# Kernel tuning notes

Measured on AMD Instinct MI355X. Metric: run time of the kernel, lower is better.

## Reference

```python
import jax, jax.numpy as jnp
import numpy as np

N = 100000      # nodes
E = 1600000     # edges
NODE_DIM = 128
HID = 128
L = 3           # num_layers
B = 512         # graphs in batch
EPS = 1e-5      # LayerNorm eps


def setup_inputs() -> dict:
    key = jax.random.key(0)
    ks = jax.random.split(key, 8)
    nodes = jax.random.normal(ks[0], (N, NODE_DIM), jnp.float32)
    edges = jax.random.randint(ks[1], (2, E), 0, N, dtype=jnp.int32)
    edge_types = jax.random.randint(ks[2], (E,), 0, 10, dtype=jnp.int32)
    batch_idx = jnp.sort(jax.random.randint(ks[3], (N,), 0, B, dtype=jnp.int32))
    w_in = jax.random.normal(ks[4], (NODE_DIM, HID), jnp.float32) / np.sqrt(NODE_DIM)
    b_in = jnp.zeros((HID,), jnp.float32)
    gcn_w = jax.random.normal(ks[5], (L, HID, HID), jnp.float32) / np.sqrt(HID)
    gcn_b = jnp.zeros((L, HID), jnp.float32)
    ln_g = jnp.ones((L, HID), jnp.float32)
    ln_b = jnp.zeros((L, HID), jnp.float32)
    return {"nodes": nodes, "edges": edges, "edge_types": edge_types,
            "batch_idx": batch_idx, "w_in": w_in, "b_in": b_in,
            "gcn_w": gcn_w, "gcn_b": gcn_b, "ln_g": ln_g, "ln_b": ln_b}


def _layer_norm(x, g, b):
    mu = jnp.mean(x, axis=-1, keepdims=True)
    var = jnp.mean(jnp.square(x - mu), axis=-1, keepdims=True)
    return (x - mu) * jax.lax.rsqrt(var + EPS) * g + b


def reference(nodes, edges, edge_types, batch_idx, w_in, b_in, gcn_w, gcn_b, ln_g, ln_b):
    src, dst = edges[0], edges[1]
    # GCN normalization with self-loops: deg = in-degree(A) + 1
    deg = jax.ops.segment_sum(jnp.ones((E,), nodes.dtype), dst, num_segments=N) + 1.0
    dinv_sqrt = jax.lax.rsqrt(deg)
    dinv = 1.0 / deg                       # self-loop norm = 1/deg_i
    enorm = dinv_sqrt[src] * dinv_sqrt[dst]

    x = nodes @ w_in + b_in                # input projection [N, HID]
    for i in range(L):
        res = x
        xw = x @ gcn_w[i]
        agg = jax.ops.segment_sum(xw[src] * enorm[:, None], dst, num_segments=N)
        x = agg + xw * dinv[:, None] + gcn_b[i]
        x = jax.nn.relu(_layer_norm(x, ln_g[i], ln_b[i]))
        # dropout is identity in eval mode
        if i > 0:
            x = x + res                    # residual only for i > 0

    # global mean pool per graph
    counts = jax.ops.segment_sum(jnp.ones((N,), x.dtype), batch_idx, num_segments=B)
    plan = jax.ops.segment_sum(x, batch_idx, num_segments=B) / jnp.maximum(counts, 1.0)[:, None]
    return x, plan
```

## Files before the change

kernel.cpp:

```cpp
#include <hip/hip_runtime.h>
#include <hip/hip_bf16.h>

typedef __attribute__((ext_vector_type(8))) short bf16x8;
typedef __attribute__((ext_vector_type(4))) float f32x4;
typedef __attribute__((ext_vector_type(2))) float f32x2;

#define K1_TILE 6144
#define NBCAP 4608

__device__ __forceinline__ unsigned short f2bf(float f) {
    union { unsigned int i; float f; } x; x.f = f;
    unsigned int r = (x.i + 0x7fffu + ((x.i >> 16) & 1u)) >> 16;
    return (unsigned short)r;
}
__device__ __forceinline__ float blo(unsigned int u) { return __uint_as_float(u << 16); }
__device__ __forceinline__ float bhi(unsigned int u) { return __uint_as_float(u & 0xffff0000u); }


__global__ __launch_bounds__(256) void bin2_k(const int* __restrict__ src,
                                              const int* __restrict__ dst,
                                              int* __restrict__ bucket_cursor,
                                              int* __restrict__ bins,
                                              int E, int NB) {
    __shared__ int hist[512];
    __shared__ int lbase[513];
    __shared__ int gdiff[512];
    __shared__ int wsum[4];
    __shared__ int stage[K1_TILE];
    int tid = threadIdx.x;
    int base = blockIdx.x * K1_TILE;
    int cnt = min(K1_TILE, E - base);

    hist[tid] = 0; hist[tid + 256] = 0;
    __syncthreads();
    for (int i = tid; i < cnt; i += 256) atomicAdd(&hist[dst[base + i] >> 8], 1);
    __syncthreads();

    int h0 = hist[2 * tid], h1 = hist[2 * tid + 1];
    int v = h0 + h1;
    int lane = tid & 63, wid = tid >> 6;
    int s = v;
#pragma unroll
    for (int o = 1; o < 64; o <<= 1) { int n = __shfl_up(s, o); if (lane >= o) s += n; }
    if (lane == 63) wsum[wid] = s;
    __syncthreads();
    if (tid == 0) { int r = 0; for (int w = 0; w < 4; ++w) { int t2 = wsum[w]; wsum[w] = r; r += t2; } }
    __syncthreads();
    int lb0 = s + wsum[wid] - v;
    int lb1 = lb0 + h0;
    int b0 = 2 * tid, b1 = 2 * tid + 1;
    int gb0 = 0, gb1 = 0;
    if (h0 > 0 && b0 < NB) gb0 = atomicAdd(&bucket_cursor[b0], h0);
    if (h1 > 0 && b1 < NB) gb1 = atomicAdd(&bucket_cursor[b1], h1);
    __syncthreads();
    hist[b0] = lb0; hist[b1] = lb1;
    lbase[b0] = lb0; lbase[b1] = lb1;
    gdiff[b0] = gb0 - lb0; gdiff[b1] = gb1 - lb1;
    if (tid == 0) lbase[512] = cnt;
    __syncthreads();

    for (int i = tid; i < cnt; i += 256) {
        int sv = src[base + i], dv = dst[base + i];
        int pos = atomicAdd(&hist[dv >> 8], 1);
        stage[pos] = ((dv & 255) << 24) | sv;
    }
    __syncthreads();

    for (int i = tid; i < cnt; i += 256) {
        int lo = 0, hi = 512;
        while (lo + 1 < hi) { int mid = (lo + hi) >> 1; if (lbase[mid] <= i) lo = mid; else hi = mid; }
        int p = gdiff[lo] + i;
        if (p < NBCAP) bins[(size_t)lo * NBCAP + p] = stage[i];
    }
}


__global__ __launch_bounds__(256) void bucket_scan_k(const int* __restrict__ bucket_cursor,
                                                     int* __restrict__ bucket_base, int NB) {
    __shared__ int wsum[4];
    int tid = threadIdx.x;
    int h0 = (2 * tid < NB) ? min(bucket_cursor[2 * tid], NBCAP) : 0;
    int h1 = (2 * tid + 1 < NB) ? min(bucket_cursor[2 * tid + 1], NBCAP) : 0;
    int v = h0 + h1;
    int lane = tid & 63, wid = tid >> 6;
    int s = v;
#pragma unroll
    for (int o = 1; o < 64; o <<= 1) { int n = __shfl_up(s, o); if (lane >= o) s += n; }
    if (lane == 63) wsum[wid] = s;
    __syncthreads();
    if (tid == 0) { int r = 0; for (int w = 0; w < 4; ++w) { int t2 = wsum[w]; wsum[w] = r; r += t2; } }
    __syncthreads();
    int excl = s + wsum[wid] - v;
    if (2 * tid < NB) bucket_base[2 * tid] = excl;
    if (2 * tid + 1 < NB) bucket_base[2 * tid + 1] = excl + h0;
}


__global__ __launch_bounds__(256) void csr_build_k(const int* __restrict__ bins,
                                                   const int* __restrict__ bucket_cursor,
                                                   const int* __restrict__ bucket_base,
                                                   int* __restrict__ csr_src,
                                                   int* __restrict__ row_start,
                                                   float* __restrict__ dinv_sqrt,
                                                   float* __restrict__ dinv,
                                                   int N) {
    __shared__ int counts[256];
    __shared__ int cursor[256];
    __shared__ int wsum[4];
    __shared__ int lcsr[NBCAP];
    int b = blockIdx.x, tid = threadIdx.x;
    int cnt = min(bucket_cursor[b], NBCAP);
    int cbase = bucket_base[b];
    const int* my = bins + (size_t)b * NBCAP;

    counts[tid] = 0;
    __syncthreads();
    for (int i = tid; i < cnt; i += 256) atomicAdd(&counts[((unsigned)my[i]) >> 24], 1);
    __syncthreads();

    int v = counts[tid];
    int lane = tid & 63, wid = tid >> 6;
    int s = v;
#pragma unroll
    for (int o = 1; o < 64; o <<= 1) { int n = __shfl_up(s, o); if (lane >= o) s += n; }
    if (lane == 63) wsum[wid] = s;
    __syncthreads();
    if (tid == 0) { int r = 0; for (int w = 0; w < 4; ++w) { int t2 = wsum[w]; wsum[w] = r; r += t2; } }
    __syncthreads();
    int excl = s + wsum[wid] - v;

    int node = b * 256 + tid;
    if (node <= N) row_start[node] = cbase + excl;
    if (node < N) {
        float dg = (float)v + 1.0f;
        dinv_sqrt[node] = rsqrtf(dg);
        dinv[node] = 1.0f / dg;
    }
    cursor[tid] = excl;
    __syncthreads();

    for (int i = tid; i < cnt; i += 256) {
        int e = my[i];
        int pos = atomicAdd(&cursor[((unsigned)e) >> 24], 1);
        lcsr[pos] = e & 0xffffff;
    }
    __syncthreads();
    for (int i = tid; i < cnt; i += 256) csr_src[cbase + i] = lcsr[i];
}


__global__ __launch_bounds__(256) void pack_w_k(const float* __restrict__ w_in,
                                                const float* __restrict__ gcn_w,
                                                unsigned short* __restrict__ Wp) {
    int t = blockIdx.x * 256 + threadIdx.x;
    if (t >= 8192) return;
    int mat = t >> 11;
    int kb = (t >> 9) & 3;
    int ct = (t >> 6) & 7;
    int lane = t & 63;
    int q = lane >> 4, c = lane & 15;
    const float* W = (mat == 0) ? w_in : (gcn_w + (size_t)(mat - 1) * 16384);
    unsigned short o[8];
#pragma unroll
    for (int j = 0; j < 8; ++j)
        o[j] = f2bf(W[(size_t)(kb * 32 + q * 8 + j) * 128 + ct * 16 + c]);
    unsigned short* dstp = Wp + ((size_t)t) * 8;
#pragma unroll
    for (int j = 0; j < 8; ++j) dstp[j] = o[j];
}


__global__ __launch_bounds__(256) void proj_k(const float* __restrict__ A,
                                              const unsigned short* __restrict__ Wp,
                                              const float* __restrict__ bias,
                                              unsigned short* __restrict__ Cb,
                                              int M) {
    __shared__ unsigned short stage[64 * 128];
    int wid = threadIdx.x >> 6, lane = threadIdx.x & 63;
    int blk0 = blockIdx.x * 64;
    int r0 = blk0 + wid * 16;
    int q = lane >> 4, c = lane & 15;
    int ar = min(r0 + c, M - 1);

    f32x4 acc[8];
#pragma unroll
    for (int ct = 0; ct < 8; ++ct) acc[ct] = (f32x4){0.f, 0.f, 0.f, 0.f};

#pragma unroll
    for (int kb = 0; kb < 4; ++kb) {
        float4 f0 = *(const float4*)&A[(size_t)ar * 128 + kb * 32 + q * 8];
        float4 f1 = *(const float4*)&A[(size_t)ar * 128 + kb * 32 + q * 8 + 4];
        union { unsigned short u[8]; bf16x8 v; } af;
        af.u[0] = f2bf(f0.x); af.u[1] = f2bf(f0.y); af.u[2] = f2bf(f0.z); af.u[3] = f2bf(f0.w);
        af.u[4] = f2bf(f1.x); af.u[5] = f2bf(f1.y); af.u[6] = f2bf(f1.z); af.u[7] = f2bf(f1.w);
#pragma unroll
        for (int ct = 0; ct < 8; ++ct) {
            bf16x8 b = *(const bf16x8*)&Wp[(((size_t)(kb * 8 + ct)) * 64 + lane) * 8];
            acc[ct] = __builtin_amdgcn_mfma_f32_16x16x32_bf16(af.v, b, acc[ct], 0, 0, 0);
        }
    }

#pragma unroll
    for (int ct = 0; ct < 8; ++ct) {
        int col = ct * 16 + c;
        float bv = bias[col];
#pragma unroll
        for (int r = 0; r < 4; ++r)
            stage[(wid * 16 + q * 4 + r) * 128 + col] = f2bf(acc[ct][r] + bv);
    }
    __syncthreads();

    int tid = threadIdx.x;
#pragma unroll
    for (int i = 0; i < 4; ++i) {
        int k = tid + i * 256;
        int row = k >> 4, colc = (k & 15) * 8;
        int grow = blk0 + row;
        if (grow < M)
            *(uint4*)&Cb[(size_t)grow * 128 + colc] = *(const uint4*)&stage[row * 128 + colc];
    }
}


__global__ __launch_bounds__(256) void gemmln_k(const unsigned short* __restrict__ S,
                                                unsigned short* xb16,
                                                float* __restrict__ xout,
                                                const unsigned short* __restrict__ Wp,
                                                const float* __restrict__ bias,
                                                const float* __restrict__ g,
                                                const float* __restrict__ bb,
                                                int M, int residual, int write_f32) {
    __shared__ unsigned short stage[64 * 128];
    int wid = threadIdx.x >> 6, lane = threadIdx.x & 63;
    int blk0 = blockIdx.x * 64;
    int r0 = blk0 + wid * 16;
    int q = lane >> 4, c = lane & 15;
    int ar = min(r0 + c, M - 1);

    f32x4 acc[8];
#pragma unroll
    for (int ct = 0; ct < 8; ++ct) acc[ct] = (f32x4){0.f, 0.f, 0.f, 0.f};

#pragma unroll
    for (int kb = 0; kb < 4; ++kb) {
        bf16x8 a = *(const bf16x8*)&S[(size_t)ar * 128 + kb * 32 + q * 8];
#pragma unroll
        for (int ct = 0; ct < 8; ++ct) {
            bf16x8 b = *(const bf16x8*)&Wp[(((size_t)(kb * 8 + ct)) * 64 + lane) * 8];
            acc[ct] = __builtin_amdgcn_mfma_f32_16x16x32_bf16(a, b, acc[ct], 0, 0, 0);
        }
    }

    float v[8][4];
#pragma unroll
    for (int ct = 0; ct < 8; ++ct) {
        float bv = bias[ct * 16 + c];
#pragma unroll
        for (int r = 0; r < 4; ++r) v[ct][r] = acc[ct][r] + bv;
    }

    float mu[4], rs[4];
#pragma unroll
    for (int r = 0; r < 4; ++r) {
        float s = 0.f;
#pragma unroll
        for (int ct = 0; ct < 8; ++ct) s += v[ct][r];
        s += __shfl_xor(s, 1); s += __shfl_xor(s, 2);
        s += __shfl_xor(s, 4); s += __shfl_xor(s, 8);
        mu[r] = s * (1.0f / 128.0f);
    }
#pragma unroll
    for (int r = 0; r < 4; ++r) {
        float s = 0.f;
#pragma unroll
        for (int ct = 0; ct < 8; ++ct) { float d = v[ct][r] - mu[r]; s += d * d; }
        s += __shfl_xor(s, 1); s += __shfl_xor(s, 2);
        s += __shfl_xor(s, 4); s += __shfl_xor(s, 8);
        rs[r] = rsqrtf(s * (1.0f / 128.0f) + 1e-5f);
    }

#pragma unroll
    for (int ct = 0; ct < 8; ++ct) {
        int col = ct * 16 + c;
        float gamma = g[col], beta = bb[col];
#pragma unroll
        for (int r = 0; r < 4; ++r) {
            float y = fmaxf((v[ct][r] - mu[r]) * rs[r] * gamma + beta, 0.f);
            stage[(wid * 16 + q * 4 + r) * 128 + col] = f2bf(y);
        }
    }
    __syncthreads();

    int tid = threadIdx.x;
#pragma unroll
    for (int i = 0; i < 4; ++i) {
        int k = tid + i * 256;
        int row = k >> 4, colc = (k & 15) * 8;
        int grow = blk0 + row;
        if (grow >= M) continue;
        uint4 sv = *(const uint4*)&stage[row * 128 + colc];
        float y0 = blo(sv.x), y1 = bhi(sv.x), y2 = blo(sv.y), y3 = bhi(sv.y);
        float y4 = blo(sv.z), y5 = bhi(sv.z), y6 = blo(sv.w), y7 = bhi(sv.w);
        if (residual) {
            uint4 rv = *(const uint4*)&xb16[(size_t)grow * 128 + colc];
            y0 += blo(rv.x); y1 += bhi(rv.x); y2 += blo(rv.y); y3 += bhi(rv.y);
            y4 += blo(rv.z); y5 += bhi(rv.z); y6 += blo(rv.w); y7 += bhi(rv.w);
        }
        union { unsigned short u[8]; uint4 qv; } o;
        o.u[0] = f2bf(y0); o.u[1] = f2bf(y1); o.u[2] = f2bf(y2); o.u[3] = f2bf(y3);
        o.u[4] = f2bf(y4); o.u[5] = f2bf(y5); o.u[6] = f2bf(y6); o.u[7] = f2bf(y7);
        *(uint4*)&xb16[(size_t)grow * 128 + colc] = o.qv;
        if (write_f32) {
            *(float4*)&xout[(size_t)grow * 128 + colc] = make_float4(y0, y1, y2, y3);
            *(float4*)&xout[(size_t)grow * 128 + colc + 4] = make_float4(y4, y5, y6, y7);
        }
    }
}


__device__ __forceinline__ void acc8(f32x2& a0, f32x2& a1, f32x2& a2, f32x2& a3,
                                     uint4 u, float w) {
    f32x2 w2 = {w, w};
    f32x2 p0 = {blo(u.x), bhi(u.x)};
    f32x2 p1 = {blo(u.y), bhi(u.y)};
    f32x2 p2 = {blo(u.z), bhi(u.z)};
    f32x2 p3 = {blo(u.w), bhi(u.w)};
    a0 += p0 * w2; a1 += p1 * w2; a2 += p2 * w2; a3 += p3 * w2;
}

__global__ __launch_bounds__(256) void agg_k(const unsigned short* __restrict__ xb16,
                                             unsigned short* __restrict__ S,
                                             const int* __restrict__ row_start,
                                             const int* __restrict__ csr_src,
                                             const float* __restrict__ dst_tbl,
                                             const float* __restrict__ dinv,
                                             int N) {
    int wid = threadIdx.x >> 6, lane = threadIdx.x & 63;
    int n = blockIdx.x * 4 + wid;
    if (n >= N) return;
    int grp = lane >> 4;
    int sl = lane & 15;
    int c0 = sl * 8;

    int beg = row_start[n], end = row_start[n + 1];
    int deg = end - beg;

    int pidx = 0; float pw = 0.f;
    if (lane < deg) {
        pidx = csr_src[beg + lane];
        pw = dst_tbl[pidx];
    }

    f32x2 a0 = {0.f, 0.f}, a1 = {0.f, 0.f}, a2 = {0.f, 0.f}, a3 = {0.f, 0.f};

    int dcap = min(deg, 64);
    for (int j = 0; j < dcap; j += 16) {
        int e0 = j + grp, e1 = e0 + 4, e2 = e0 + 8, e3 = e0 + 12;
        int s0 = __shfl(pidx, e0); float w0 = __shfl(pw, e0);
        int s1 = __shfl(pidx, e1); float w1 = __shfl(pw, e1);
        int s2 = __shfl(pidx, e2); float w2 = __shfl(pw, e2);
        int s3 = __shfl(pidx, e3); float w3 = __shfl(pw, e3);
        uint4 u0 = *(const uint4*)(xb16 + (s0 * 128 + c0));
        uint4 u1 = *(const uint4*)(xb16 + (s1 * 128 + c0));
        uint4 u2 = *(const uint4*)(xb16 + (s2 * 128 + c0));
        uint4 u3 = *(const uint4*)(xb16 + (s3 * 128 + c0));
        acc8(a0, a1, a2, a3, u0, w0);
        acc8(a0, a1, a2, a3, u1, w1);
        acc8(a0, a1, a2, a3, u2, w2);
        acc8(a0, a1, a2, a3, u3, w3);
    }

    for (int j = 64; j < deg; j += 8) {
        int ja = j + grp, jb = j + grp + 4;
        int sa = csr_src[beg + min(ja, deg - 1)];
        int sb = csr_src[beg + min(jb, deg - 1)];
        float wa = (ja < deg) ? dst_tbl[sa] : 0.f;
        float wb = (jb < deg) ? dst_tbl[sb] : 0.f;
        uint4 ua = *(const uint4*)(xb16 + (sa * 128 + c0));
        uint4 ub = *(const uint4*)(xb16 + (sb * 128 + c0));
        acc8(a0, a1, a2, a3, ua, wa);
        acc8(a0, a1, a2, a3, ub, wb);
    }

#pragma unroll
    for (int o = 16; o <= 32; o <<= 1) {
        a0.x += __shfl_xor(a0.x, o); a0.y += __shfl_xor(a0.y, o);
        a1.x += __shfl_xor(a1.x, o); a1.y += __shfl_xor(a1.y, o);
        a2.x += __shfl_xor(a2.x, o); a2.y += __shfl_xor(a2.y, o);
        a3.x += __shfl_xor(a3.x, o); a3.y += __shfl_xor(a3.y, o);
    }

    if (grp == 0) {
        float dsd = dst_tbl[n];
        float di = dinv[n];
        uint4 u = *(const uint4*)(xb16 + (n * 128 + c0));
        float y0 = a0.x * dsd + blo(u.x) * di;
        float y1 = a0.y * dsd + bhi(u.x) * di;
        float y2 = a1.x * dsd + blo(u.y) * di;
        float y3 = a1.y * dsd + bhi(u.y) * di;
        float y4 = a2.x * dsd + blo(u.z) * di;
        float y5 = a2.y * dsd + bhi(u.z) * di;
        float y6 = a3.x * dsd + blo(u.w) * di;
        float y7 = a3.y * dsd + bhi(u.w) * di;
        union { unsigned short us[8]; uint4 qv; } o;
        o.us[0] = f2bf(y0); o.us[1] = f2bf(y1); o.us[2] = f2bf(y2); o.us[3] = f2bf(y3);
        o.us[4] = f2bf(y4); o.us[5] = f2bf(y5); o.us[6] = f2bf(y6); o.us[7] = f2bf(y7);
        *(uint4*)(S + (n * 128 + c0)) = o.qv;
    }
}


__global__ __launch_bounds__(256) void bounds_k(const int* __restrict__ bidx,
                                                int* __restrict__ gstart, int N, int B) {
    int i = blockIdx.x * 256 + threadIdx.x;
    if (i > N) return;
    int cur = (i < N) ? bidx[i] : B;
    int prev = (i == 0) ? -1 : bidx[i - 1];
    for (int b = prev + 1; b <= cur; ++b) gstart[b] = i;
}

__global__ __launch_bounds__(256) void pool_k(const unsigned short* __restrict__ x,
                                              const int* __restrict__ gstart,
                                              float* __restrict__ plan) {
    __shared__ float red[8 * 128];
    int b = blockIdx.x, t = threadIdx.x;
    int cg = (t & 31) * 4;
    int h = t >> 5;
    int s = gstart[b], e = gstart[b + 1];
    float acc0 = 0.f, acc1 = 0.f, acc2 = 0.f, acc3 = 0.f;
    for (int i = s + h; i < e; i += 8) {
        uint2 u = *(const uint2*)&x[(size_t)i * 128 + cg];
        acc0 += blo(u.x); acc1 += bhi(u.x); acc2 += blo(u.y); acc3 += bhi(u.y);
    }
    red[h * 128 + cg] = acc0; red[h * 128 + cg + 1] = acc1;
    red[h * 128 + cg + 2] = acc2; red[h * 128 + cg + 3] = acc3;
    __syncthreads();
    if (h == 0) {
#pragma unroll
        for (int k = 1; k < 8; ++k) {
            acc0 += red[k * 128 + cg];     acc1 += red[k * 128 + cg + 1];
            acc2 += red[k * 128 + cg + 2]; acc3 += red[k * 128 + cg + 3];
        }
        float inv = 1.0f / (float)max(e - s, 1);
        *(float4*)&plan[(size_t)b * 128 + cg] = make_float4(acc0 * inv, acc1 * inv,
                                                            acc2 * inv, acc3 * inv);
    }
}


extern "C" void kernel_launch(void* const* d_in, const int* in_sizes, int n_in,
                              void* d_out, int out_size, void* d_ws, size_t ws_size,
                              hipStream_t stream) {
    const float* nodes     = (const float*)d_in[0];
    const int*   edges     = (const int*)d_in[1];
    const int*   batch_idx = (const int*)d_in[3];
    const float* w_in      = (const float*)d_in[4];
    const float* b_in      = (const float*)d_in[5];
    const float* gcn_w     = (const float*)d_in[6];
    const float* gcn_b     = (const float*)d_in[7];
    const float* ln_g      = (const float*)d_in[8];
    const float* ln_b      = (const float*)d_in[9];

    const int N = in_sizes[0] / 128;
    const int E = in_sizes[1] / 2;
    const int B = out_size / 128 - N;
    const int* src = edges;
    const int* dst = edges + E;
    const int NB = (N + 256) / 256;

    float* xbuf = (float*)d_out;
    float* plan = xbuf + (size_t)N * 128;

    unsigned short* xb16 = (unsigned short*)d_ws;
    unsigned short* Sb   = xb16 + (size_t)N * 128;
    unsigned short* Wp   = Sb + (size_t)N * 128;
    int* bins            = (int*)(Wp + 4 * 16384);
    int* bucket_cursor   = bins + (size_t)NB * NBCAP;
    int* bucket_base     = bucket_cursor + NB;
    int* csr_src         = bucket_base + NB;
    int* row_start       = csr_src + E;
    float* dinv_sqrt     = (float*)(row_start + N + 1);
    float* dinv          = dinv_sqrt + N;
    int* gstart          = (int*)(dinv + N);

    hipMemsetAsync(bucket_cursor, 0, sizeof(int) * NB, stream);

    bin2_k<<<(E + K1_TILE - 1) / K1_TILE, 256, 0, stream>>>(src, dst, bucket_cursor, bins, E, NB);
    bucket_scan_k<<<1, 256, 0, stream>>>(bucket_cursor, bucket_base, NB);
    csr_build_k<<<NB, 256, 0, stream>>>(bins, bucket_cursor, bucket_base,
                                        csr_src, row_start, dinv_sqrt, dinv, N);

    pack_w_k<<<32, 256, 0, stream>>>(w_in, gcn_w, Wp);

    proj_k<<<(N + 63) / 64, 256, 0, stream>>>(nodes, Wp, b_in, xb16, N);

    for (int l = 0; l < 3; ++l) {
        agg_k<<<(N + 3) / 4, 256, 0, stream>>>(xb16, Sb, row_start, csr_src,
                                               dinv_sqrt, dinv, N);
        gemmln_k<<<(N + 63) / 64, 256, 0, stream>>>(Sb, xb16, xbuf,
                                                    Wp + (size_t)(l + 1) * 16384,
                                                    gcn_b + (size_t)l * 128,
                                                    ln_g + (size_t)l * 128,
                                                    ln_b + (size_t)l * 128, N,
                                                    l > 0 ? 1 : 0, l == 2 ? 1 : 0);
    }

    bounds_k<<<(N + 1 + 255) / 256, 256, 0, stream>>>(batch_idx, gstart, N, B);
    pool_k<<<B, 256, 0, stream>>>(xb16, gstart, plan);
}
```

Measured before the change: 454.4 us.

## Recast neighbor aggregation as MFMA sparse-block matmul with self-loops in CSR

Adds each node's self-loop as an explicit CSR entry and precomputes per-edge bf16 source weights, so the self term no longer needs the separate dinv path. The aggregation kernel now processes 16 destination nodes per wave: it gathers 32-edge chunks of source rows into LDS, builds a masked weight matrix, and accumulates with bf16 MFMA instead of scalar FMA shuffles. The goal is better gather coalescing and compute throughput. In exchange it does wasted MFMA work on mostly-zero masks, adds an extra preprocessing kernel, and rounds the edge weights and self-loop contribution to bf16.

```diff
diff --git a/kernel.cpp b/kernel.cpp
--- a/kernel.cpp
+++ b/kernel.cpp
@@ -3,7 +3,6 @@
 
 typedef __attribute__((ext_vector_type(8))) short bf16x8;
 typedef __attribute__((ext_vector_type(4))) float f32x4;
-typedef __attribute__((ext_vector_type(2))) float f32x2;
 
 #define K1_TILE 6144
 #define NBCAP 4608
@@ -76,11 +75,14 @@
 
 
 __global__ __launch_bounds__(256) void bucket_scan_k(const int* __restrict__ bucket_cursor,
-                                                     int* __restrict__ bucket_base, int NB) {
+                                                     int* __restrict__ bucket_base,
+                                                     int NB, int N) {
     __shared__ int wsum[4];
     int tid = threadIdx.x;
-    int h0 = (2 * tid < NB) ? min(bucket_cursor[2 * tid], NBCAP) : 0;
-    int h1 = (2 * tid + 1 < NB) ? min(bucket_cursor[2 * tid + 1], NBCAP) : 0;
+    int nc0 = max(0, min(256, N - (2 * tid) * 256));
+    int nc1 = max(0, min(256, N - (2 * tid + 1) * 256));
+    int h0 = (2 * tid < NB) ? min(bucket_cursor[2 * tid], NBCAP) + nc0 : 0;
+    int h1 = (2 * tid + 1 < NB) ? min(bucket_cursor[2 * tid + 1], NBCAP) + nc1 : 0;
     int v = h0 + h1;
     int lane = tid & 63, wid = tid >> 6;
     int s = v;
@@ -102,14 +104,14 @@
                                                    int* __restrict__ csr_src,
                                                    int* __restrict__ row_start,
                                                    float* __restrict__ dinv_sqrt,
-                                                   float* __restrict__ dinv,
                                                    int N) {
     __shared__ int counts[256];
     __shared__ int cursor[256];
     __shared__ int wsum[4];
-    __shared__ int lcsr[NBCAP];
+    __shared__ int lcsr[NBCAP + 256];
     int b = blockIdx.x, tid = threadIdx.x;
     int cnt = min(bucket_cursor[b], NBCAP);
+    int nodecnt = max(0, min(256, N - b * 256));
     int cbase = bucket_base[b];
     const int* my = bins + (size_t)b * NBCAP;
 
@@ -118,25 +120,26 @@
     for (int i = tid; i < cnt; i += 256) atomicAdd(&counts[((unsigned)my[i]) >> 24], 1);
     __syncthreads();
 
+    int node = b * 256 + tid;
     int v = counts[tid];
+    int sz = (node < N) ? v + 1 : 0;
     int lane = tid & 63, wid = tid >> 6;
-    int s = v;
+    int s = sz;
 #pragma unroll
     for (int o = 1; o < 64; o <<= 1) { int n = __shfl_up(s, o); if (lane >= o) s += n; }
     if (lane == 63) wsum[wid] = s;
     __syncthreads();
     if (tid == 0) { int r = 0; for (int w = 0; w < 4; ++w) { int t2 = wsum[w]; wsum[w] = r; r += t2; } }
     __syncthreads();
-    int excl = s + wsum[wid] - v;
-
-    int node = b * 256 + tid;
+    int excl = s + wsum[wid] - sz;
+
     if (node <= N) row_start[node] = cbase + excl;
     if (node < N) {
         float dg = (float)v + 1.0f;
         dinv_sqrt[node] = rsqrtf(dg);
-        dinv[node] = 1.0f / dg;
-    }
-    cursor[tid] = excl;
+        lcsr[excl] = node;
+    }
+    cursor[tid] = excl + ((node < N) ? 1 : 0);
     __syncthreads();
 
     for (int i = tid; i < cnt; i += 256) {
@@ -145,7 +148,20 @@
         lcsr[pos] = e & 0xffffff;
     }
     __syncthreads();
-    for (int i = tid; i < cnt; i += 256) csr_src[cbase + i] = lcsr[i];
+    int cnt_total = cnt + nodecnt;
+    for (int i = tid; i < cnt_total; i += 256) csr_src[cbase + i] = lcsr[i];
+}
+
+
+__global__ __launch_bounds__(256) void wbf_k(const int* __restrict__ csr_src,
+                                             const float* __restrict__ dinv_sqrt,
+                                             unsigned short* __restrict__ wbf,
+                                             int total, int N) {
+    int i = blockIdx.x * 256 + threadIdx.x;
+    if (i >= total) return;
+    int s = csr_src[i];
+    s = min(max(s, 0), N - 1);
+    wbf[i] = f2bf(dinv_sqrt[s]);
 }
 
 
@@ -318,94 +334,109 @@
 }
 
 
-__device__ __forceinline__ void acc8(f32x2& a0, f32x2& a1, f32x2& a2, f32x2& a3,
-                                     uint4 u, float w) {
-    f32x2 w2 = {w, w};
-    f32x2 p0 = {blo(u.x), bhi(u.x)};
-    f32x2 p1 = {blo(u.y), bhi(u.y)};
-    f32x2 p2 = {blo(u.z), bhi(u.z)};
-    f32x2 p3 = {blo(u.w), bhi(u.w)};
-    a0 += p0 * w2; a1 += p1 * w2; a2 += p2 * w2; a3 += p3 * w2;
-}
+#define AST 36
+#define ATILE (64 * AST)
 
 __global__ __launch_bounds__(256) void agg_k(const unsigned short* __restrict__ xb16,
                                              unsigned short* __restrict__ S,
                                              const int* __restrict__ row_start,
                                              const int* __restrict__ csr_src,
-                                             const float* __restrict__ dst_tbl,
-                                             const float* __restrict__ dinv,
+                                             const unsigned short* __restrict__ wbf,
+                                             const float* __restrict__ dinv_sqrt,
                                              int N) {
+    __shared__ unsigned int lds[4 * ATILE];
     int wid = threadIdx.x >> 6, lane = threadIdx.x & 63;
-    int n = blockIdx.x * 4 + wid;
-    if (n >= N) return;
-    int grp = lane >> 4;
-    int sl = lane & 15;
-    int c0 = sl * 8;
-
-    int beg = row_start[n], end = row_start[n + 1];
-    int deg = end - beg;
-
-    int pidx = 0; float pw = 0.f;
-    if (lane < deg) {
-        pidx = csr_src[beg + lane];
-        pw = dst_tbl[pidx];
-    }
-
-    f32x2 a0 = {0.f, 0.f}, a1 = {0.f, 0.f}, a2 = {0.f, 0.f}, a3 = {0.f, 0.f};
-
-    int dcap = min(deg, 64);
-    for (int j = 0; j < dcap; j += 16) {
-        int e0 = j + grp, e1 = e0 + 4, e2 = e0 + 8, e3 = e0 + 12;
-        int s0 = __shfl(pidx, e0); float w0 = __shfl(pw, e0);
-        int s1 = __shfl(pidx, e1); float w1 = __shfl(pw, e1);
-        int s2 = __shfl(pidx, e2); float w2 = __shfl(pw, e2);
-        int s3 = __shfl(pidx, e3); float w3 = __shfl(pw, e3);
-        uint4 u0 = *(const uint4*)(xb16 + (s0 * 128 + c0));
-        uint4 u1 = *(const uint4*)(xb16 + (s1 * 128 + c0));
-        uint4 u2 = *(const uint4*)(xb16 + (s2 * 128 + c0));
-        uint4 u3 = *(const uint4*)(xb16 + (s3 * 128 + c0));
-        acc8(a0, a1, a2, a3, u0, w0);
-        acc8(a0, a1, a2, a3, u1, w1);
-        acc8(a0, a1, a2, a3, u2, w2);
-        acc8(a0, a1, a2, a3, u3, w3);
-    }
-
-    for (int j = 64; j < deg; j += 8) {
-        int ja = j + grp, jb = j + grp + 4;
-        int sa = csr_src[beg + min(ja, deg - 1)];
-        int sb = csr_src[beg + min(jb, deg - 1)];
-        float wa = (ja < deg) ? dst_tbl[sa] : 0.f;
-        float wb = (jb < deg) ? dst_tbl[sb] : 0.f;
-        uint4 ua = *(const uint4*)(xb16 + (sa * 128 + c0));
-        uint4 ub = *(const uint4*)(xb16 + (sb * 128 + c0));
-        acc8(a0, a1, a2, a3, ua, wa);
-        acc8(a0, a1, a2, a3, ub, wb);
-    }
-
-#pragma unroll
-    for (int o = 16; o <= 32; o <<= 1) {
-        a0.x += __shfl_xor(a0.x, o); a0.y += __shfl_xor(a0.y, o);
-        a1.x += __shfl_xor(a1.x, o); a1.y += __shfl_xor(a1.y, o);
-        a2.x += __shfl_xor(a2.x, o); a2.y += __shfl_xor(a2.y, o);
-        a3.x += __shfl_xor(a3.x, o); a3.y += __shfl_xor(a3.y, o);
-    }
-
-    if (grp == 0) {
-        float dsd = dst_tbl[n];
-        float di = dinv[n];
-        uint4 u = *(const uint4*)(xb16 + (n * 128 + c0));
-        float y0 = a0.x * dsd + blo(u.x) * di;
-        float y1 = a0.y * dsd + bhi(u.x) * di;
-        float y2 = a1.x * dsd + blo(u.y) * di;
-        float y3 = a1.y * dsd + bhi(u.y) * di;
-        float y4 = a2.x * dsd + blo(u.z) * di;
-        float y5 = a2.y * dsd + bhi(u.z) * di;
-        float y6 = a3.x * dsd + blo(u.w) * di;
-        float y7 = a3.y * dsd + bhi(u.w) * di;
-        union { unsigned short us[8]; uint4 qv; } o;
-        o.us[0] = f2bf(y0); o.us[1] = f2bf(y1); o.us[2] = f2bf(y2); o.us[3] = f2bf(y3);
-        o.us[4] = f2bf(y4); o.us[5] = f2bf(y5); o.us[6] = f2bf(y6); o.us[7] = f2bf(y7);
-        *(uint4*)(S + (n * 128 + c0)) = o.qv;
+    int ngroups = (N + 15) >> 4;
+    int g = blockIdx.x * 4 + wid;
+    if (g >= ngroups) return;
+    int n0 = g << 4;
+    unsigned int* T = lds + wid * ATILE;
+
+    int q = lane >> 4, c = lane & 15;
+
+    int nc = n0 + c;
+    int rs_lo = 0, rs_hi = 0;
+    if (nc < N) { rs_lo = row_start[nc]; rs_hi = row_start[nc + 1]; }
+    int beg  = row_start[n0];
+    int endp = row_start[min(n0 + 16, N)];
+    int kb = beg & ~31;
+    int nch = (endp - kb + 31) >> 5;
+
+    unsigned sel = (c & 1) ? 0x07060302u : 0x05040100u;
+    int xsw = (c & 3) << 3;
+
+    f32x4 acc[8];
+#pragma unroll
+    for (int ct = 0; ct < 8; ++ct) acc[ct] = (f32x4){0.f, 0.f, 0.f, 0.f};
+
+    for (int ch = 0; ch < nch; ++ch) {
+        int kbase = kb + (ch << 5);
+
+        uint4 st[8];
+#pragma unroll
+        for (int it = 0; it < 8; ++it) {
+            int s = csr_src[kbase + it * 4 + q];
+            s = min(max(s, 0), N - 1);
+            st[it] = *(const uint4*)&xb16[(size_t)s * 128 + c * 8];
+        }
+
+        const uint4 wv = *(const uint4*)&wbf[kbase + q * 8];
+        int gk0 = kbase + q * 8;
+        int jlo = min(max(rs_lo - gk0, 0), 8);
+        int jhi = min(max(rs_hi - gk0, 0), 8);
+        union { unsigned u[4]; bf16x8 v; } bA;
+#pragma unroll
+        for (int d = 0; d < 4; ++d) {
+            int j0 = 2 * d, j1 = 2 * d + 1;
+            unsigned m = ((j0 >= jlo && j0 < jhi) ? 0x0000ffffu : 0u) |
+                         ((j1 >= jlo && j1 < jhi) ? 0xffff0000u : 0u);
+            bA.u[d] = ((const unsigned*)&wv)[d] & m;
+        }
+
+#pragma unroll
+        for (int it = 0; it < 8; ++it) {
+            int kx = (it * 4 + q) ^ xsw;
+            T[(c * 4 + 0) * AST + kx] = st[it].x;
+            T[(c * 4 + 1) * AST + kx] = st[it].y;
+            T[(c * 4 + 2) * AST + kx] = st[it].z;
+            T[(c * 4 + 3) * AST + kx] = st[it].w;
+        }
+        asm volatile("s_waitcnt lgkmcnt(0)" ::: "memory");
+
+#pragma unroll
+        for (int ct = 0; ct < 8; ++ct) {
+            int ch2r = ct * 8 + (c >> 1);
+            int sr = (ch2r >> 2) & 3;
+            int cb = ch2r * AST + ((q ^ sr) << 3);
+            const uint4 A0 = *(const uint4*)&T[cb];
+            const uint4 A1 = *(const uint4*)&T[cb + 4];
+            union { unsigned u[4]; bf16x8 v; } bB;
+            bB.u[0] = __builtin_amdgcn_perm(A0.y, A0.x, sel);
+            bB.u[1] = __builtin_amdgcn_perm(A0.w, A0.z, sel);
+            bB.u[2] = __builtin_amdgcn_perm(A1.y, A1.x, sel);
+            bB.u[3] = __builtin_amdgcn_perm(A1.w, A1.z, sel);
+            acc[ct] = __builtin_amdgcn_mfma_f32_16x16x32_bf16(bA.v, bB.v, acc[ct], 0, 0, 0);
+        }
+        asm volatile("s_waitcnt lgkmcnt(0)" ::: "memory");
+    }
+
+    unsigned short* my = (unsigned short*)T;
+    float dsd[4];
+#pragma unroll
+    for (int r = 0; r < 4; ++r) dsd[r] = dinv_sqrt[min(n0 + q * 4 + r, N - 1)];
+#pragma unroll
+    for (int ct = 0; ct < 8; ++ct)
+#pragma unroll
+        for (int r = 0; r < 4; ++r)
+            my[(q * 4 + r) * 128 + ct * 16 + c] = f2bf(acc[ct][r] * dsd[r]);
+    asm volatile("s_waitcnt lgkmcnt(0)" ::: "memory");
+#pragma unroll
+    for (int it = 0; it < 4; ++it) {
+        int k2 = it * 64 + lane;
+        int row = k2 >> 4, off = (k2 & 15) * 8;
+        int nn = n0 + row;
+        if (nn < N)
+            *(uint4*)&S[(size_t)nn * 128 + off] = *(const uint4*)&my[row * 128 + off];
     }
 }
 
@@ -467,6 +498,7 @@
     const int* src = edges;
     const int* dst = edges + E;
     const int NB = (N + 256) / 256;
+    const int CSRLEN = E + N + 64;
 
     float* xbuf = (float*)d_out;
     float* plan = xbuf + (size_t)N * 128;
@@ -475,28 +507,30 @@
     unsigned short* Sb   = xb16 + (size_t)N * 128;
     unsigned short* Wp   = Sb + (size_t)N * 128;
     int* bins            = (int*)(Wp + 4 * 16384);
+    unsigned short* wbf  = (unsigned short*)bins;
     int* bucket_cursor   = bins + (size_t)NB * NBCAP;
     int* bucket_base     = bucket_cursor + NB;
     int* csr_src         = bucket_base + NB;
-    int* row_start       = csr_src + E;
+    int* row_start       = csr_src + CSRLEN;
     float* dinv_sqrt     = (float*)(row_start + N + 1);
-    float* dinv          = dinv_sqrt + N;
-    int* gstart          = (int*)(dinv + N);
+    int* gstart          = (int*)(dinv_sqrt + N);
 
     hipMemsetAsync(bucket_cursor, 0, sizeof(int) * NB, stream);
 
     bin2_k<<<(E + K1_TILE - 1) / K1_TILE, 256, 0, stream>>>(src, dst, bucket_cursor, bins, E, NB);
-    bucket_scan_k<<<1, 256, 0, stream>>>(bucket_cursor, bucket_base, NB);
+    bucket_scan_k<<<1, 256, 0, stream>>>(bucket_cursor, bucket_base, NB, N);
     csr_build_k<<<NB, 256, 0, stream>>>(bins, bucket_cursor, bucket_base,
-                                        csr_src, row_start, dinv_sqrt, dinv, N);
+                                        csr_src, row_start, dinv_sqrt, N);
+    wbf_k<<<(E + N + 255) / 256, 256, 0, stream>>>(csr_src, dinv_sqrt, wbf, E + N, N);
 
     pack_w_k<<<32, 256, 0, stream>>>(w_in, gcn_w, Wp);
 
     proj_k<<<(N + 63) / 64, 256, 0, stream>>>(nodes, Wp, b_in, xb16, N);
 
+    const int ngroups = (N + 15) / 16;
     for (int l = 0; l < 3; ++l) {
-        agg_k<<<(N + 3) / 4, 256, 0, stream>>>(xb16, Sb, row_start, csr_src,
-                                               dinv_sqrt, dinv, N);
+        agg_k<<<(ngroups + 3) / 4, 256, 0, stream>>>(xb16, Sb, row_start, csr_src,
+                                                     wbf, dinv_sqrt, N);
         gemmln_k<<<(N + 63) / 64, 256, 0, stream>>>(Sb, xb16, xbuf,
                                                     Wp + (size_t)(l + 1) * 16384,
                                                     gcn_b + (size_t)l * 128,
```

Result: slower. 492.8 us (+8.5%).

## Fuse neighbor aggregation with GEMM+LayerNorm into one kernel per layer

Applied to the files above, without the earlier changes.

Merges the per-node gather aggregation and the MFMA GEMM+LayerNorm+ReLU+residual into a single kernel. Each 64-row block aggregates its 16 rows per wave into padded LDS, then runs the GEMM straight from LDS. This drops the bf16 S intermediate round trip through global memory and one launch per layer. Because the output can no longer be written in place, it ping-pongs between two activation buffers. In exchange, each wave now walks 16 nodes serially, which gives far fewer waves (about 1.5k blocks instead of 25k) to hide gather latency.

```diff
diff --git a/kernel.cpp b/kernel.cpp
--- a/kernel.cpp
+++ b/kernel.cpp
@@ -7,6 +7,7 @@
 
 #define K1_TILE 6144
 #define NBCAP 4608
+#define PAD 136
 
 __device__ __forceinline__ unsigned short f2bf(float f) {
     union { unsigned int i; float f; } x; x.f = f;
@@ -222,102 +223,6 @@
 }
 
 
-__global__ __launch_bounds__(256) void gemmln_k(const unsigned short* __restrict__ S,
-                                                unsigned short* xb16,
-                                                float* __restrict__ xout,
-                                                const unsigned short* __restrict__ Wp,
-                                                const float* __restrict__ bias,
-                                                const float* __restrict__ g,
-                                                const float* __restrict__ bb,
-                                                int M, int residual, int write_f32) {
-    __shared__ unsigned short stage[64 * 128];
-    int wid = threadIdx.x >> 6, lane = threadIdx.x & 63;
-    int blk0 = blockIdx.x * 64;
-    int r0 = blk0 + wid * 16;
-    int q = lane >> 4, c = lane & 15;
-    int ar = min(r0 + c, M - 1);
-
-    f32x4 acc[8];
-#pragma unroll
-    for (int ct = 0; ct < 8; ++ct) acc[ct] = (f32x4){0.f, 0.f, 0.f, 0.f};
-
-#pragma unroll
-    for (int kb = 0; kb < 4; ++kb) {
-        bf16x8 a = *(const bf16x8*)&S[(size_t)ar * 128 + kb * 32 + q * 8];
-#pragma unroll
-        for (int ct = 0; ct < 8; ++ct) {
-            bf16x8 b = *(const bf16x8*)&Wp[(((size_t)(kb * 8 + ct)) * 64 + lane) * 8];
-            acc[ct] = __builtin_amdgcn_mfma_f32_16x16x32_bf16(a, b, acc[ct], 0, 0, 0);
-        }
-    }
-
-    float v[8][4];
-#pragma unroll
-    for (int ct = 0; ct < 8; ++ct) {
-        float bv = bias[ct * 16 + c];
-#pragma unroll
-        for (int r = 0; r < 4; ++r) v[ct][r] = acc[ct][r] + bv;
-    }
-
-    float mu[4], rs[4];
-#pragma unroll
-    for (int r = 0; r < 4; ++r) {
-        float s = 0.f;
-#pragma unroll
-        for (int ct = 0; ct < 8; ++ct) s += v[ct][r];
-        s += __shfl_xor(s, 1); s += __shfl_xor(s, 2);
-        s += __shfl_xor(s, 4); s += __shfl_xor(s, 8);
-        mu[r] = s * (1.0f / 128.0f);
-    }
-#pragma unroll
-    for (int r = 0; r < 4; ++r) {
-        float s = 0.f;
-#pragma unroll
-        for (int ct = 0; ct < 8; ++ct) { float d = v[ct][r] - mu[r]; s += d * d; }
-        s += __shfl_xor(s, 1); s += __shfl_xor(s, 2);
-        s += __shfl_xor(s, 4); s += __shfl_xor(s, 8);
-        rs[r] = rsqrtf(s * (1.0f / 128.0f) + 1e-5f);
-    }
-
-#pragma unroll
-    for (int ct = 0; ct < 8; ++ct) {
-        int col = ct * 16 + c;
-        float gamma = g[col], beta = bb[col];
-#pragma unroll
-        for (int r = 0; r < 4; ++r) {
-            float y = fmaxf((v[ct][r] - mu[r]) * rs[r] * gamma + beta, 0.f);
-            stage[(wid * 16 + q * 4 + r) * 128 + col] = f2bf(y);
-        }
-    }
-    __syncthreads();
-
-    int tid = threadIdx.x;
-#pragma unroll
-    for (int i = 0; i < 4; ++i) {
-        int k = tid + i * 256;
-        int row = k >> 4, colc = (k & 15) * 8;
-        int grow = blk0 + row;
-        if (grow >= M) continue;
-        uint4 sv = *(const uint4*)&stage[row * 128 + colc];
-        float y0 = blo(sv.x), y1 = bhi(sv.x), y2 = blo(sv.y), y3 = bhi(sv.y);
-        float y4 = blo(sv.z), y5 = bhi(sv.z), y6 = blo(sv.w), y7 = bhi(sv.w);
-        if (residual) {
-            uint4 rv = *(const uint4*)&xb16[(size_t)grow * 128 + colc];
-            y0 += blo(rv.x); y1 += bhi(rv.x); y2 += blo(rv.y); y3 += bhi(rv.y);
-            y4 += blo(rv.z); y5 += bhi(rv.z); y6 += blo(rv.w); y7 += bhi(rv.w);
-        }
-        union { unsigned short u[8]; uint4 qv; } o;
-        o.u[0] = f2bf(y0); o.u[1] = f2bf(y1); o.u[2] = f2bf(y2); o.u[3] = f2bf(y3);
-        o.u[4] = f2bf(y4); o.u[5] = f2bf(y5); o.u[6] = f2bf(y6); o.u[7] = f2bf(y7);
-        *(uint4*)&xb16[(size_t)grow * 128 + colc] = o.qv;
-        if (write_f32) {
-            *(float4*)&xout[(size_t)grow * 128 + colc] = make_float4(y0, y1, y2, y3);
-            *(float4*)&xout[(size_t)grow * 128 + colc + 4] = make_float4(y4, y5, y6, y7);
-        }
-    }
-}
-
-
 __device__ __forceinline__ void acc8(f32x2& a0, f32x2& a1, f32x2& a2, f32x2& a3,
                                      uint4 u, float w) {
     f32x2 w2 = {w, w};
@@ -328,84 +233,176 @@
     a0 += p0 * w2; a1 += p1 * w2; a2 += p2 * w2; a3 += p3 * w2;
 }
 
-__global__ __launch_bounds__(256) void agg_k(const unsigned short* __restrict__ xb16,
-                                             unsigned short* __restrict__ S,
-                                             const int* __restrict__ row_start,
-                                             const int* __restrict__ csr_src,
-                                             const float* __restrict__ dst_tbl,
-                                             const float* __restrict__ dinv,
-                                             int N) {
+__global__ __launch_bounds__(256) void aggemm_k(const unsigned short* __restrict__ xin,
+                                                unsigned short* __restrict__ xout,
+                                                float* __restrict__ xf32,
+                                                const int* __restrict__ row_start,
+                                                const int* __restrict__ csr_src,
+                                                const float* __restrict__ dst_tbl,
+                                                const float* __restrict__ dinv,
+                                                const unsigned short* __restrict__ Wp,
+                                                const float* __restrict__ bias,
+                                                const float* __restrict__ g,
+                                                const float* __restrict__ bb,
+                                                int N, int residual, int write_f32) {
+    __shared__ unsigned short stage[64 * PAD];
     int wid = threadIdx.x >> 6, lane = threadIdx.x & 63;
-    int n = blockIdx.x * 4 + wid;
-    if (n >= N) return;
-    int grp = lane >> 4;
-    int sl = lane & 15;
+    int blk0 = blockIdx.x * 64;
+    int nbase = blk0 + wid * 16;
+    int grp = lane >> 4, sl = lane & 15;
     int c0 = sl * 8;
 
-    int beg = row_start[n], end = row_start[n + 1];
-    int deg = end - beg;
-
-    int pidx = 0; float pw = 0.f;
-    if (lane < deg) {
-        pidx = csr_src[beg + lane];
-        pw = dst_tbl[pidx];
-    }
-
-    f32x2 a0 = {0.f, 0.f}, a1 = {0.f, 0.f}, a2 = {0.f, 0.f}, a3 = {0.f, 0.f};
-
-    int dcap = min(deg, 64);
-    for (int j = 0; j < dcap; j += 16) {
-        int e0 = j + grp, e1 = e0 + 4, e2 = e0 + 8, e3 = e0 + 12;
-        int s0 = __shfl(pidx, e0); float w0 = __shfl(pw, e0);
-        int s1 = __shfl(pidx, e1); float w1 = __shfl(pw, e1);
-        int s2 = __shfl(pidx, e2); float w2 = __shfl(pw, e2);
-        int s3 = __shfl(pidx, e3); float w3 = __shfl(pw, e3);
-        uint4 u0 = *(const uint4*)(xb16 + (s0 * 128 + c0));
-        uint4 u1 = *(const uint4*)(xb16 + (s1 * 128 + c0));
-        uint4 u2 = *(const uint4*)(xb16 + (s2 * 128 + c0));
-        uint4 u3 = *(const uint4*)(xb16 + (s3 * 128 + c0));
-        acc8(a0, a1, a2, a3, u0, w0);
-        acc8(a0, a1, a2, a3, u1, w1);
-        acc8(a0, a1, a2, a3, u2, w2);
-        acc8(a0, a1, a2, a3, u3, w3);
-    }
-
-    for (int j = 64; j < deg; j += 8) {
-        int ja = j + grp, jb = j + grp + 4;
-        int sa = csr_src[beg + min(ja, deg - 1)];
-        int sb = csr_src[beg + min(jb, deg - 1)];
-        float wa = (ja < deg) ? dst_tbl[sa] : 0.f;
-        float wb = (jb < deg) ? dst_tbl[sb] : 0.f;
-        uint4 ua = *(const uint4*)(xb16 + (sa * 128 + c0));
-        uint4 ub = *(const uint4*)(xb16 + (sb * 128 + c0));
-        acc8(a0, a1, a2, a3, ua, wa);
-        acc8(a0, a1, a2, a3, ub, wb);
-    }
-
-#pragma unroll
-    for (int o = 16; o <= 32; o <<= 1) {
-        a0.x += __shfl_xor(a0.x, o); a0.y += __shfl_xor(a0.y, o);
-        a1.x += __shfl_xor(a1.x, o); a1.y += __shfl_xor(a1.y, o);
-        a2.x += __shfl_xor(a2.x, o); a2.y += __shfl_xor(a2.y, o);
-        a3.x += __shfl_xor(a3.x, o); a3.y += __shfl_xor(a3.y, o);
-    }
-
-    if (grp == 0) {
-        float dsd = dst_tbl[n];
-        float di = dinv[n];
-        uint4 u = *(const uint4*)(xb16 + (n * 128 + c0));
-        float y0 = a0.x * dsd + blo(u.x) * di;
-        float y1 = a0.y * dsd + bhi(u.x) * di;
-        float y2 = a1.x * dsd + blo(u.y) * di;
-        float y3 = a1.y * dsd + bhi(u.y) * di;
-        float y4 = a2.x * dsd + blo(u.z) * di;
-        float y5 = a2.y * dsd + bhi(u.z) * di;
-        float y6 = a3.x * dsd + blo(u.w) * di;
-        float y7 = a3.y * dsd + bhi(u.w) * di;
-        union { unsigned short us[8]; uint4 qv; } o;
-        o.us[0] = f2bf(y0); o.us[1] = f2bf(y1); o.us[2] = f2bf(y2); o.us[3] = f2bf(y3);
-        o.us[4] = f2bf(y4); o.us[5] = f2bf(y5); o.us[6] = f2bf(y6); o.us[7] = f2bf(y7);
-        *(uint4*)(S + (n * 128 + c0)) = o.qv;
+    int rsv = 0;
+    if (lane < 17) rsv = row_start[min(nbase + lane, N)];
+
+    for (int i = 0; i < 16; ++i) {
+        int n = nbase + i;
+        int beg = __shfl(rsv, i), end = __shfl(rsv, i + 1);
+        if (n >= N) continue;
+        int deg = end - beg;
+
+        int pidx = 0; float pw = 0.f;
+        if (lane < deg) {
+            pidx = csr_src[beg + lane];
+            pw = dst_tbl[pidx];
+        }
+
+        f32x2 a0 = {0.f, 0.f}, a1 = {0.f, 0.f}, a2 = {0.f, 0.f}, a3 = {0.f, 0.f};
+        int dcap = min(deg, 64);
+        for (int j = 0; j < dcap; j += 16) {
+            int e0 = j + grp, e1 = e0 + 4, e2 = e0 + 8, e3 = e0 + 12;
+            int s0 = __shfl(pidx, e0); float w0 = __shfl(pw, e0);
+            int s1 = __shfl(pidx, e1); float w1 = __shfl(pw, e1);
+            int s2 = __shfl(pidx, e2); float w2 = __shfl(pw, e2);
+            int s3 = __shfl(pidx, e3); float w3 = __shfl(pw, e3);
+            uint4 u0 = *(const uint4*)(xin + (s0 * 128 + c0));
+            uint4 u1 = *(const uint4*)(xin + (s1 * 128 + c0));
+            uint4 u2 = *(const uint4*)(xin + (s2 * 128 + c0));
+            uint4 u3 = *(const uint4*)(xin + (s3 * 128 + c0));
+            acc8(a0, a1, a2, a3, u0, w0);
+            acc8(a0, a1, a2, a3, u1, w1);
+            acc8(a0, a1, a2, a3, u2, w2);
+            acc8(a0, a1, a2, a3, u3, w3);
+        }
+        for (int j = 64; j < deg; j += 8) {
+            int ja = j + grp, jb = j + grp + 4;
+            int sa = csr_src[beg + min(ja, deg - 1)];
+            int sb = csr_src[beg + min(jb, deg - 1)];
+            float wa = (ja < deg) ? dst_tbl[sa] : 0.f;
+            float wb = (jb < deg) ? dst_tbl[sb] : 0.f;
+            uint4 ua = *(const uint4*)(xin + (sa * 128 + c0));
+            uint4 ub = *(const uint4*)(xin + (sb * 128 + c0));
+            acc8(a0, a1, a2, a3, ua, wa);
+            acc8(a0, a1, a2, a3, ub, wb);
+        }
+
+#pragma unroll
+        for (int o = 16; o <= 32; o <<= 1) {
+            a0.x += __shfl_xor(a0.x, o); a0.y += __shfl_xor(a0.y, o);
+            a1.x += __shfl_xor(a1.x, o); a1.y += __shfl_xor(a1.y, o);
+            a2.x += __shfl_xor(a2.x, o); a2.y += __shfl_xor(a2.y, o);
+            a3.x += __shfl_xor(a3.x, o); a3.y += __shfl_xor(a3.y, o);
+        }
+
+        if (grp == 0) {
+            float dsd = dst_tbl[n];
+            float di = dinv[n];
+            uint4 u = *(const uint4*)(xin + (n * 128 + c0));
+            float y0 = a0.x * dsd + blo(u.x) * di;
+            float y1 = a0.y * dsd + bhi(u.x) * di;
+            float y2 = a1.x * dsd + blo(u.y) * di;
+            float y3 = a1.y * dsd + bhi(u.y) * di;
+            float y4 = a2.x * dsd + blo(u.z) * di;
+            float y5 = a2.y * dsd + bhi(u.z) * di;
+            float y6 = a3.x * dsd + blo(u.w) * di;
+            float y7 = a3.y * dsd + bhi(u.w) * di;
+            union { unsigned short us[8]; uint4 qv; } o;
+            o.us[0] = f2bf(y0); o.us[1] = f2bf(y1); o.us[2] = f2bf(y2); o.us[3] = f2bf(y3);
+            o.us[4] = f2bf(y4); o.us[5] = f2bf(y5); o.us[6] = f2bf(y6); o.us[7] = f2bf(y7);
+            *(uint4*)&stage[(wid * 16 + i) * PAD + c0] = o.qv;
+        }
+    }
+    __syncthreads();
+
+    int q = lane >> 4, c = lane & 15;
+
+    f32x4 acc[8];
+#pragma unroll
+    for (int ct = 0; ct < 8; ++ct) acc[ct] = (f32x4){0.f, 0.f, 0.f, 0.f};
+
+#pragma unroll
+    for (int kb = 0; kb < 4; ++kb) {
+        bf16x8 a = *(const bf16x8*)&stage[(wid * 16 + c) * PAD + kb * 32 + q * 8];
+#pragma unroll
+        for (int ct = 0; ct < 8; ++ct) {
+            bf16x8 b = *(const bf16x8*)&Wp[(((size_t)(kb * 8 + ct)) * 64 + lane) * 8];
+            acc[ct] = __builtin_amdgcn_mfma_f32_16x16x32_bf16(a, b, acc[ct], 0, 0, 0);
+        }
+    }
+
+    float v[8][4];
+#pragma unroll
+    for (int ct = 0; ct < 8; ++ct) {
+        float bv = bias[ct * 16 + c];
+#pragma unroll
+        for (int r = 0; r < 4; ++r) v[ct][r] = acc[ct][r] + bv;
+    }
+
+    float mu[4], rs[4];
+#pragma unroll
+    for (int r = 0; r < 4; ++r) {
+        float s = 0.f;
+#pragma unroll
+        for (int ct = 0; ct < 8; ++ct) s += v[ct][r];
+        s += __shfl_xor(s, 1); s += __shfl_xor(s, 2);
+        s += __shfl_xor(s, 4); s += __shfl_xor(s, 8);
+        mu[r] = s * (1.0f / 128.0f);
+    }
+#pragma unroll
+    for (int r = 0; r < 4; ++r) {
+        float s = 0.f;
+#pragma unroll
+        for (int ct = 0; ct < 8; ++ct) { float d = v[ct][r] - mu[r]; s += d * d; }
+        s += __shfl_xor(s, 1); s += __shfl_xor(s, 2);
+        s += __shfl_xor(s, 4); s += __shfl_xor(s, 8);
+        rs[r] = rsqrtf(s * (1.0f / 128.0f) + 1e-5f);
+    }
+
+#pragma unroll
+    for (int ct = 0; ct < 8; ++ct) {
+        int col = ct * 16 + c;
+        float gamma = g[col], beta = bb[col];
+#pragma unroll
+        for (int r = 0; r < 4; ++r) {
+            float y = fmaxf((v[ct][r] - mu[r]) * rs[r] * gamma + beta, 0.f);
+            stage[(wid * 16 + q * 4 + r) * PAD + col] = f2bf(y);
+        }
+    }
+    __syncthreads();
+
+    int tid = threadIdx.x;
+#pragma unroll
+    for (int i = 0; i < 4; ++i) {
+        int k = tid + i * 256;
+        int row = k >> 4, colc = (k & 15) * 8;
+        int grow = blk0 + row;
+        if (grow >= N) continue;
+        uint4 sv = *(const uint4*)&stage[row * PAD + colc];
+        float y0 = blo(sv.x), y1 = bhi(sv.x), y2 = blo(sv.y), y3 = bhi(sv.y);
+        float y4 = blo(sv.z), y5 = bhi(sv.z), y6 = blo(sv.w), y7 = bhi(sv.w);
+        if (residual) {
+            uint4 rv = *(const uint4*)&xin[(size_t)grow * 128 + colc];
+            y0 += blo(rv.x); y1 += bhi(rv.x); y2 += blo(rv.y); y3 += bhi(rv.y);
+            y4 += blo(rv.z); y5 += bhi(rv.z); y6 += blo(rv.w); y7 += bhi(rv.w);
+        }
+        union { unsigned short u[8]; uint4 qv; } o;
+        o.u[0] = f2bf(y0); o.u[1] = f2bf(y1); o.u[2] = f2bf(y2); o.u[3] = f2bf(y3);
+        o.u[4] = f2bf(y4); o.u[5] = f2bf(y5); o.u[6] = f2bf(y6); o.u[7] = f2bf(y7);
+        *(uint4*)&xout[(size_t)grow * 128 + colc] = o.qv;
+        if (write_f32) {
+            *(float4*)&xf32[(size_t)grow * 128 + colc] = make_float4(y0, y1, y2, y3);
+            *(float4*)&xf32[(size_t)grow * 128 + colc + 4] = make_float4(y4, y5, y6, y7);
+        }
     }
 }
 
@@ -471,9 +468,9 @@
     float* xbuf = (float*)d_out;
     float* plan = xbuf + (size_t)N * 128;
 
-    unsigned short* xb16 = (unsigned short*)d_ws;
-    unsigned short* Sb   = xb16 + (size_t)N * 128;
-    unsigned short* Wp   = Sb + (size_t)N * 128;
+    unsigned short* xa   = (unsigned short*)d_ws;
+    unsigned short* xb   = xa + (size_t)N * 128;
+    unsigned short* Wp   = xb + (size_t)N * 128;
     int* bins            = (int*)(Wp + 4 * 16384);
     int* bucket_cursor   = bins + (size_t)NB * NBCAP;
     int* bucket_base     = bucket_cursor + NB;
@@ -492,19 +489,21 @@
 
     pack_w_k<<<32, 256, 0, stream>>>(w_in, gcn_w, Wp);
 
-    proj_k<<<(N + 63) / 64, 256, 0, stream>>>(nodes, Wp, b_in, xb16, N);
-
+    proj_k<<<(N + 63) / 64, 256, 0, stream>>>(nodes, Wp, b_in, xa, N);
+
+    const int nblk = (N + 63) / 64;
     for (int l = 0; l < 3; ++l) {
-        agg_k<<<(N + 3) / 4, 256, 0, stream>>>(xb16, Sb, row_start, csr_src,
-                                               dinv_sqrt, dinv, N);
-        gemmln_k<<<(N + 63) / 64, 256, 0, stream>>>(Sb, xb16, xbuf,
-                                                    Wp + (size_t)(l + 1) * 16384,
-                                                    gcn_b + (size_t)l * 128,
-                                                    ln_g + (size_t)l * 128,
-                                                    ln_b + (size_t)l * 128, N,
-                                                    l > 0 ? 1 : 0, l == 2 ? 1 : 0);
+        unsigned short* xin  = (l & 1) ? xb : xa;
+        unsigned short* xout = (l & 1) ? xa : xb;
+        aggemm_k<<<nblk, 256, 0, stream>>>(xin, xout, xbuf, row_start, csr_src,
+                                           dinv_sqrt, dinv,
+                                           Wp + (size_t)(l + 1) * 16384,
+                                           gcn_b + (size_t)l * 128,
+                                           ln_g + (size_t)l * 128,
+                                           ln_b + (size_t)l * 128, N,
+                                           l > 0 ? 1 : 0, l == 2 ? 1 : 0);
     }
 
     bounds_k<<<(N + 1 + 255) / 256, 256, 0, stream>>>(batch_idx, gstart, N, B);
-    pool_k<<<B, 256, 0, stream>>>(xb16, gstart, plan);
-}
+    pool_k<<<B, 256, 0, stream>>>(xb, gstart, plan);
+}
```

Result: no change. 457.1 us (+0.6%).
